# Kernel optimization log

Measured on AMD Instinct MI355X. Metric: run time of the kernel, lower is better.

Reference implementation:

```python
import jax, jax.numpy as jnp
import numpy as np

N_CHUNKS = 4 * 28  # hardcoded 112 chunks in the original; chunk sizes are equal when N % 112 == 0


def setup_inputs() -> dict:
    key = jax.random.key(0)
    k1, k2, k3 = jax.random.split(key, 3)
    b, d, h, w = 8, 512, 28, 28  # N = b*h*w = 6272, divisible by 112
    x = jax.random.normal(k1, (b, d, h, w), dtype=jnp.float32)
    p_mu = jax.random.normal(k2, (b * h * w, d), dtype=jnp.float32)
    p_logvar = jax.random.normal(k3, (b * h * w, d), dtype=jnp.float32)
    return {"x": x, "p_mu": p_mu, "p_logvar": p_logvar}


def _club_loss(x, p_mu, p_logvar):
    # (b, d, h, w) -> (N, d) with N = b*h*w
    b, d, h, w = x.shape
    flat_x = jnp.transpose(x, (0, 2, 3, 1)).reshape(-1, d)  # (N, d)

    inv_ev = jnp.exp(-p_logvar)  # (N, d)

    # positive[i] = -0.5 * sum_d (x_i - mu_i)^2 / exp(logvar_i)
    positive = -0.5 * jnp.sum(jnp.square(flat_x - p_mu) * inv_ev, axis=-1)  # (N,)

    # negative[i] = -0.5 * mean_j sum_d (x_j - mu_i)^2 / exp(logvar_i)
    # Expand the square so the j-contraction becomes GEMMs (no (N,N,d) intermediate):
    #   D[i,j] = <x_j^2, inv_ev_i> - 2 <x_j, mu_i * inv_ev_i> + <mu_i^2, inv_ev_i>
    x2 = jnp.square(flat_x)                                   # (N, d)
    term_x2 = jnp.einsum('id,jd->ij', inv_ev, x2)             # (N_i, N_j)
    term_cross = jnp.einsum('id,jd->ij', p_mu * inv_ev, flat_x)
    term_mu2 = jnp.sum(jnp.square(p_mu) * inv_ev, axis=-1, keepdims=True)  # (N_i, 1)
    D = term_x2 - 2.0 * term_cross + term_mu2                 # (N_i, N_j)
    negative = -0.5 * jnp.mean(D, axis=1)                     # (N,)

    # Original averages each of the 112 equal-size chunks then averages the
    # chunk means, which equals the global mean for equal chunk sizes.
    return jnp.mean(positive - negative)


def reference(x, p_mu, p_logvar):
    return _club_loss(x, p_mu, p_logvar)
```

## Files before the change

kernel.cpp:

```cpp
#include <hip/hip_runtime.h>


#define Dd   512
#define HWs  784
#define Nn   6272
#define NBLK 448


__global__ __launch_bounds__(256) void club_all(
    const float* __restrict__ x, const float* __restrict__ p_mu,
    const float* __restrict__ p_lv, float* __restrict__ ws,
    float* __restrict__ out)
{
    __shared__ float sbuf[16];
    __shared__ int lastFlag;
    __shared__ double redd[256];

    const int t     = threadIdx.x;
    const int blk   = blockIdx.x;
    const int b     = blk / 56;
    const int rem   = blk % 56;
    const int half  = rem & 1;
    const int chunk = rem >> 1;
    const int hw0   = chunk * 28;
    const int c     = 256 * half + t;
    const int r0    = b * HWs + hw0;
    const int rep   = blk & 7;

    const float* xr = x + ((size_t)(b * Dd + c) * HWs + hw0);
    const float* mp = p_mu + (size_t)r0 * Dd + c;
    const float* lp = p_lv + (size_t)r0 * Dd + c;

    float sI = 0.f, sM = 0.f, sX = 0.f, sX2 = 0.f, aP = 0.f, aM2 = 0.f;

#pragma unroll
    for (int k = 0; k < 7; ++k) {
        const float4 xq = *(const float4*)(xr + 4 * k);
        const float xv0 = xq.x, xv1 = xq.y, xv2 = xq.z, xv3 = xq.w;
#define STEP(J, XV) do {                                               \
        const size_t ro = (size_t)(4 * k + (J)) * Dd;                  \
        const float mu = mp[ro];                                       \
        const float lv = lp[ro];                                       \
        const float iev = __expf(-lv);                                 \
        const float dd = (XV) - mu;                                    \
        aP += dd * dd * iev;                                           \
        sI += iev;                                                     \
        const float mi = mu * iev;                                     \
        sM += mi; aM2 += mu * mi;                                      \
        sX += (XV); sX2 += (XV) * (XV);                                \
    } while (0)
        STEP(0, xv0); STEP(1, xv1); STEP(2, xv2); STEP(3, xv3);
#undef STEP
    }

#pragma unroll
    for (int off = 32; off > 0; off >>= 1) {
        aP  += __shfl_down(aP,  off);
        aM2 += __shfl_down(aM2, off);
    }
    if ((t & 63) == 0) { sbuf[t >> 6] = aP; sbuf[8 + (t >> 6)] = aM2; }
    __syncthreads();

    atomicAdd(&ws[         rep * Dd + c], sI);
    atomicAdd(&ws[ 4096 + rep * Dd + c], sM);
    atomicAdd(&ws[ 8192 + rep * Dd + c], sX);
    atomicAdd(&ws[12288 + rep * Dd + c], sX2);
    if (t == 0) {
        double* wd = (double*)((char*)ws + 65536);
        atomicAdd(wd + rep,     (double)(sbuf[0] + sbuf[1] + sbuf[2] + sbuf[3]));
        atomicAdd(wd + 8 + rep, (double)(sbuf[8] + sbuf[9] + sbuf[10] + sbuf[11]));
    }

    if (t == 0) {
        __threadfence();
        unsigned* ctr = (unsigned*)((char*)ws + 65664);
        lastFlag = (atomicAdd(ctr, 1u) == NBLK - 1);
    }
    __syncthreads();
    if (!lastFlag) return;

    __threadfence();
    double dc = 0.0;
#pragma unroll
    for (int hh = 0; hh < 2; ++hh) {
        const int cc = t + 256 * hh;
        double vI = 0.0, vM = 0.0, vX = 0.0, v2 = 0.0;
#pragma unroll
        for (int r = 0; r < 8; ++r) {
            vI += (double)__hip_atomic_load(ws +         r * Dd + cc, __ATOMIC_RELAXED, __HIP_MEMORY_SCOPE_AGENT);
            vM += (double)__hip_atomic_load(ws +  4096 + r * Dd + cc, __ATOMIC_RELAXED, __HIP_MEMORY_SCOPE_AGENT);
            vX += (double)__hip_atomic_load(ws +  8192 + r * Dd + cc, __ATOMIC_RELAXED, __HIP_MEMORY_SCOPE_AGENT);
            v2 += (double)__hip_atomic_load(ws + 12288 + r * Dd + cc, __ATOMIC_RELAXED, __HIP_MEMORY_SCOPE_AGENT);
        }
        dc += v2 * vI - 2.0 * vX * vM;
    }
    redd[t] = dc; __syncthreads();
    for (int s = 128; s > 0; s >>= 1) {
        if (t < s) redd[t] += redd[t + s];
        __syncthreads();
    }
    if (t == 0) {
        double* wd = (double*)((char*)ws + 65536);
        double P = 0.0, M2 = 0.0;
#pragma unroll
        for (int r = 0; r < 8; ++r) {
            P  += __hip_atomic_load(wd + r,     __ATOMIC_RELAXED, __HIP_MEMORY_SCOPE_AGENT);
            M2 += __hip_atomic_load(wd + 8 + r, __ATOMIC_RELAXED, __HIP_MEMORY_SCOPE_AGENT);
        }
        const double sumD = redd[0] + (double)Nn * M2;
        out[0] = (float)((-0.5 / (double)Nn) * P
                       + (0.5 / ((double)Nn * (double)Nn)) * sumD);
    }
}

extern "C" void kernel_launch(void* const* d_in, const int* in_sizes, int n_in,
                              void* d_out, int out_size, void* d_ws, size_t ws_size,
                              hipStream_t stream) {
    const float* x    = (const float*)d_in[0];
    const float* p_mu = (const float*)d_in[1];
    const float* p_lv = (const float*)d_in[2];
    float* ws = (float*)d_ws;

    hipMemsetAsync(d_ws, 0, 65668, stream);
    club_all<<<NBLK, 256, 0, stream>>>(x, p_mu, p_lv, ws, (float*)d_out);
}
```

Before: 103.7 us.

## Use more blocks with smaller chunks and preload all row loads up front

Splits the work into 784 blocks of 16 spatial positions instead of 448 blocks of 28, and issues all 16 mu and logvar loads before computing, to raise memory-level parallelism in this latency-bound reduction. The atomic replica count grows from 8 to 64 to reduce contention. In exchange, the workspace memset becomes larger and the final block must serially reduce eight times more partial sums.

```diff
diff --git a/kernel.cpp b/kernel.cpp
--- a/kernel.cpp
+++ b/kernel.cpp
@@ -4,7 +4,8 @@
 #define Dd   512
 #define HWs  784
 #define Nn   6272
-#define NBLK 448
+#define NBLK 784
+#define REP  64
 
 
 __global__ __launch_bounds__(256) void club_all(
@@ -18,39 +19,41 @@
 
     const int t     = threadIdx.x;
     const int blk   = blockIdx.x;
-    const int b     = blk / 56;
-    const int rem   = blk % 56;
+    const int b     = blk / 98;
+    const int rem   = blk % 98;
     const int half  = rem & 1;
     const int chunk = rem >> 1;
-    const int hw0   = chunk * 28;
+    const int hw0   = chunk * 16;
     const int c     = 256 * half + t;
     const int r0    = b * HWs + hw0;
-    const int rep   = blk & 7;
+    const int rep   = blk & (REP - 1);
 
     const float* xr = x + ((size_t)(b * Dd + c) * HWs + hw0);
+    const float4 xq0 = *(const float4*)(xr + 0);
+    const float4 xq1 = *(const float4*)(xr + 4);
+    const float4 xq2 = *(const float4*)(xr + 8);
+    const float4 xq3 = *(const float4*)(xr + 12);
+
     const float* mp = p_mu + (size_t)r0 * Dd + c;
     const float* lp = p_lv + (size_t)r0 * Dd + c;
+    float mu[16], lv[16];
+#pragma unroll
+    for (int j = 0; j < 16; ++j) mu[j] = mp[(size_t)j * Dd];
+#pragma unroll
+    for (int j = 0; j < 16; ++j) lv[j] = lp[(size_t)j * Dd];
 
     float sI = 0.f, sM = 0.f, sX = 0.f, sX2 = 0.f, aP = 0.f, aM2 = 0.f;
-
+    float xv[16] = {xq0.x, xq0.y, xq0.z, xq0.w, xq1.x, xq1.y, xq1.z, xq1.w,
+                    xq2.x, xq2.y, xq2.z, xq2.w, xq3.x, xq3.y, xq3.z, xq3.w};
 #pragma unroll
-    for (int k = 0; k < 7; ++k) {
-        const float4 xq = *(const float4*)(xr + 4 * k);
-        const float xv0 = xq.x, xv1 = xq.y, xv2 = xq.z, xv3 = xq.w;
-#define STEP(J, XV) do {                                               \
-        const size_t ro = (size_t)(4 * k + (J)) * Dd;                  \
-        const float mu = mp[ro];                                       \
-        const float lv = lp[ro];                                       \
-        const float iev = __expf(-lv);                                 \
-        const float dd = (XV) - mu;                                    \
-        aP += dd * dd * iev;                                           \
-        sI += iev;                                                     \
-        const float mi = mu * iev;                                     \
-        sM += mi; aM2 += mu * mi;                                      \
-        sX += (XV); sX2 += (XV) * (XV);                                \
-    } while (0)
-        STEP(0, xv0); STEP(1, xv1); STEP(2, xv2); STEP(3, xv3);
-#undef STEP
+    for (int j = 0; j < 16; ++j) {
+        const float iev = __expf(-lv[j]);
+        const float dd  = xv[j] - mu[j];
+        aP += dd * dd * iev;
+        sI += iev;
+        const float mi = mu[j] * iev;
+        sM += mi; aM2 += mu[j] * mi;
+        sX += xv[j]; sX2 += xv[j] * xv[j];
     }
 
 #pragma unroll
@@ -61,19 +64,19 @@
     if ((t & 63) == 0) { sbuf[t >> 6] = aP; sbuf[8 + (t >> 6)] = aM2; }
     __syncthreads();
 
-    atomicAdd(&ws[         rep * Dd + c], sI);
-    atomicAdd(&ws[ 4096 + rep * Dd + c], sM);
-    atomicAdd(&ws[ 8192 + rep * Dd + c], sX);
-    atomicAdd(&ws[12288 + rep * Dd + c], sX2);
+    atomicAdd(&ws[(0 * REP + rep) * Dd + c], sI);
+    atomicAdd(&ws[(1 * REP + rep) * Dd + c], sM);
+    atomicAdd(&ws[(2 * REP + rep) * Dd + c], sX);
+    atomicAdd(&ws[(3 * REP + rep) * Dd + c], sX2);
     if (t == 0) {
-        double* wd = (double*)((char*)ws + 65536);
-        atomicAdd(wd + rep,     (double)(sbuf[0] + sbuf[1] + sbuf[2] + sbuf[3]));
-        atomicAdd(wd + 8 + rep, (double)(sbuf[8] + sbuf[9] + sbuf[10] + sbuf[11]));
+        double* wd = (double*)((char*)ws + 524288);
+        atomicAdd(wd + rep,       (double)(sbuf[0] + sbuf[1] + sbuf[2] + sbuf[3]));
+        atomicAdd(wd + REP + rep, (double)(sbuf[8] + sbuf[9] + sbuf[10] + sbuf[11]));
     }
 
     if (t == 0) {
         __threadfence();
-        unsigned* ctr = (unsigned*)((char*)ws + 65664);
+        unsigned* ctr = (unsigned*)((char*)ws + 525312);
         lastFlag = (atomicAdd(ctr, 1u) == NBLK - 1);
     }
     __syncthreads();
@@ -85,12 +88,11 @@
     for (int hh = 0; hh < 2; ++hh) {
         const int cc = t + 256 * hh;
         double vI = 0.0, vM = 0.0, vX = 0.0, v2 = 0.0;
-#pragma unroll
-        for (int r = 0; r < 8; ++r) {
-            vI += (double)__hip_atomic_load(ws +         r * Dd + cc, __ATOMIC_RELAXED, __HIP_MEMORY_SCOPE_AGENT);
-            vM += (double)__hip_atomic_load(ws +  4096 + r * Dd + cc, __ATOMIC_RELAXED, __HIP_MEMORY_SCOPE_AGENT);
-            vX += (double)__hip_atomic_load(ws +  8192 + r * Dd + cc, __ATOMIC_RELAXED, __HIP_MEMORY_SCOPE_AGENT);
-            v2 += (double)__hip_atomic_load(ws + 12288 + r * Dd + cc, __ATOMIC_RELAXED, __HIP_MEMORY_SCOPE_AGENT);
+        for (int r = 0; r < REP; ++r) {
+            vI += (double)__hip_atomic_load(ws + (0 * REP + r) * Dd + cc, __ATOMIC_RELAXED, __HIP_MEMORY_SCOPE_AGENT);
+            vM += (double)__hip_atomic_load(ws + (1 * REP + r) * Dd + cc, __ATOMIC_RELAXED, __HIP_MEMORY_SCOPE_AGENT);
+            vX += (double)__hip_atomic_load(ws + (2 * REP + r) * Dd + cc, __ATOMIC_RELAXED, __HIP_MEMORY_SCOPE_AGENT);
+            v2 += (double)__hip_atomic_load(ws + (3 * REP + r) * Dd + cc, __ATOMIC_RELAXED, __HIP_MEMORY_SCOPE_AGENT);
         }
         dc += v2 * vI - 2.0 * vX * vM;
     }
@@ -100,12 +102,12 @@
         __syncthreads();
     }
     if (t == 0) {
-        double* wd = (double*)((char*)ws + 65536);
+        double* wd = (double*)((char*)ws + 524288);
         double P = 0.0, M2 = 0.0;
 #pragma unroll
-        for (int r = 0; r < 8; ++r) {
-            P  += __hip_atomic_load(wd + r,     __ATOMIC_RELAXED, __HIP_MEMORY_SCOPE_AGENT);
-            M2 += __hip_atomic_load(wd + 8 + r, __ATOMIC_RELAXED, __HIP_MEMORY_SCOPE_AGENT);
+        for (int r = 0; r < REP; ++r) {
+            P  += __hip_atomic_load(wd + r,       __ATOMIC_RELAXED, __HIP_MEMORY_SCOPE_AGENT);
+            M2 += __hip_atomic_load(wd + REP + r, __ATOMIC_RELAXED, __HIP_MEMORY_SCOPE_AGENT);
         }
         const double sumD = redd[0] + (double)Nn * M2;
         out[0] = (float)((-0.5 / (double)Nn) * P
@@ -121,6 +123,6 @@
     const float* p_lv = (const float*)d_in[2];
     float* ws = (float*)d_ws;
 
-    hipMemsetAsync(d_ws, 0, 65668, stream);
+    hipMemsetAsync(d_ws, 0, 525316, stream);
     club_all<<<NBLK, 256, 0, stream>>>(x, p_mu, p_lv, ws, (float*)d_out);
 }
```

New measurement: 119.9 us. 15.6% more time.
